# Kernel optimization log

Hardware: AMD Instinct MI355X
Metric: run time of the kernel (lower is better)

## Reference

```python
import jax, jax.numpy as jnp
import numpy as np

EPS = 1e-10
LN_EPS = 1e-5
NEG = -1e30
H = 8  # attention_head


def _layernorm(x, g, b):
    mu = jnp.mean(x, axis=-1, keepdims=True)
    var = jnp.mean(jnp.square(x - mu), axis=-1, keepdims=True)
    return (x - mu) * jax.lax.rsqrt(var + LN_EPS) * g + b


def setup_inputs() -> dict:
    key = jax.random.key(0)
    ks = jax.random.split(key, 10)
    B, T, D = 4, 1024, 1024
    inputs = jax.random.normal(ks[0], (B, T, D), dtype=jnp.float32)
    lengths = jax.random.randint(ks[1], (B,), T // 2, T + 1).astype(jnp.int32)
    lengths = lengths.at[0].set(T)  # at least one full-length sequence
    noise_u = jax.random.uniform(ks[2], (B, H, T, T), dtype=jnp.float32)
    w = lambda k: (jax.random.normal(k, (D, D), dtype=jnp.float32) * 0.02)
    return {
        'inputs': inputs, 'lengths': lengths, 'noise_u': noise_u,
        'Wq': w(ks[3]), 'Wk': w(ks[4]), 'Wv': w(ks[5]),
        'Weq': w(ks[6]), 'Wek': w(ks[7]), 'Wfc': w(ks[8]),
        'bfc': jnp.zeros((D,), jnp.float32),
        'ln1_g': jnp.ones((D,), jnp.float32), 'ln1_b': jnp.zeros((D,), jnp.float32),
        'ln2_g': jnp.ones((D,), jnp.float32), 'ln2_b': jnp.zeros((D,), jnp.float32),
    }


def reference(inputs, lengths, noise_u, Wq, Wk, Wv, Weq, Wek, Wfc, bfc,
              ln1_g, ln1_b, ln2_g, ln2_b):
    B, T, D = inputs.shape
    dh = D // H
    # length mask: True where padded
    pad = jnp.arange(T)[None, :] >= lengths[:, None]            # (B, T)
    x = jnp.where(pad[:, :, None], 0.0, inputs)                  # zero padded positions

    def heads(W):
        h = x @ W.T                                              # (B,T,D)
        return h.reshape(B, T, H, dh).transpose(0, 2, 1, 3)      # (B,H,T,dh)

    q, k, v, eq, ek = (heads(W) for W in (Wq, Wk, Wv, Weq, Wek))
    scores = jnp.einsum('bhqd,bhkd->bhqk', q, k) / jnp.sqrt(jnp.float32(D))
    edge = jnp.einsum('bhqd,bhkd->bhqk', eq, ek)                 # (B,H,T,T)

    # bernoulli prior: binary-concrete sample (hard threshold), tau=1
    edges_prob = jax.nn.sigmoid(edge)
    logistic = jnp.log(noise_u + EPS) - jnp.log(1.0 - noise_u + EPS)
    y_soft = jax.nn.sigmoid(jnp.log(edges_prob + EPS) - jnp.log(1.0 - edges_prob + EPS) + logistic)
    gate = y_soft > 0.5                                          # hard edges (condition only, as in torch .data)

    valid = gate & (~pad[:, None, None, :])                      # gate AND key-length mask
    s = jnp.where(valid, scores, NEG)
    attn = jax.nn.softmax(s, axis=-1)
    attn = jnp.where(jnp.any(valid, axis=-1, keepdims=True), attn, 0.0)  # nan->0 for fully-masked rows

    ctx = jax.nn.relu(jnp.einsum('bhqk,bhkd->bhqd', attn, v))
    ctx = ctx.transpose(0, 2, 1, 3).reshape(B, T, D)

    h1 = _layernorm(ctx + x, ln1_g, ln1_b)
    h2 = jax.nn.relu(h1 @ Wfc.T + bfc) + h1
    out = _layernorm(h2, ln2_g, ln2_b)
    out = jnp.where(pad[:, :, None], 0.0, out)
    return out, attn, edges_prob
```

## Files before the change

### kernel.cpp

```cpp
#include <hip/hip_runtime.h>
#include <math.h>

constexpr int Bn = 4, Tn = 1024, Dn = 1024, Hn = 8, DH = 128;
constexpr float EPSF = 1e-10f;
constexpr float LN_EPSF = 1e-5f;
constexpr float NEGF = -1e30f;

typedef __attribute__((ext_vector_type(8))) short bf16x8;
typedef __attribute__((ext_vector_type(4))) float f32x4;
typedef __attribute__((ext_vector_type(4))) unsigned uint4v;

#define MFMA16(a, b, c) __builtin_amdgcn_mfma_f32_16x16x32_bf16(a, b, c, 0, 0, 0)

__device__ __forceinline__ short f2bf(float f) {
    unsigned u = __builtin_bit_cast(unsigned, f);
    u += 0x7fffu + ((u >> 16) & 1u);
    return (short)(u >> 16);
}
__device__ __forceinline__ float bf2f(short h) {
    return __builtin_bit_cast(float, ((unsigned)(unsigned short)h) << 16);
}
__device__ __forceinline__ unsigned pack2(float a, float b) {
    return ((unsigned)(unsigned short)f2bf(a)) | (((unsigned)(unsigned short)f2bf(b)) << 16);
}

__device__ __forceinline__ void gload16(const void* g, void* l) {
    __builtin_amdgcn_global_load_lds((__attribute__((address_space(1))) void*)g,
                                     (__attribute__((address_space(3))) void*)l,
                                     16, 0, 0);
}

template <int NW>
__device__ __forceinline__ void stage_b(const short* g, int ld, short* lds, int lane, int wid) {
#pragma unroll
    for (int s = 0; s < 8 / NW; ++s) {
        const int ii = wid * (8 / NW) + s;
        const int c = ii * 64 + lane;
        const int kb = c >> 7, r = c & 127;
        gload16(g + (size_t)r * ld + kb * 8, lds + ii * 512);
    }
}

template <int NW>
__device__ __forceinline__ void stage_f(const float* g, int ld, float* lds, int lane, int wid) {
#pragma unroll
    for (int s = 0; s < 16 / NW; ++s) {
        const int ii = wid * (16 / NW) + s;
        const int c = ii * 64 + lane;
        const int kb = c >> 8, half = (c >> 7) & 1, r = c & 127;
        gload16(g + (size_t)r * ld + kb * 8 + half * 4, lds + ii * 256);
    }
}

__device__ __forceinline__ bf16x8 fragb(const short* lds, int kbl, int r) {
    return *reinterpret_cast<const bf16x8*>(lds + kbl * 1024 + r * 8);
}

__device__ __forceinline__ bf16x8 fragf(const float* lds, int kbl, int r) {
    const f32x4 lo = *reinterpret_cast<const f32x4*>(lds + kbl * 1024 + r * 4);
    const f32x4 hi = *reinterpret_cast<const f32x4*>(lds + kbl * 1024 + 512 + r * 4);
    uint4v p;
    p[0] = pack2(lo[0], lo[1]);
    p[1] = pack2(lo[2], lo[3]);
    p[2] = pack2(hi[0], hi[1]);
    p[3] = pack2(hi[2], hi[3]);
    return __builtin_bit_cast(bf16x8, p);
}

struct CvtP { const float* src[6]; short* hi; short* lo; };

__global__ __launch_bounds__(256) void cvt_w(CvtP p) {
    const int i = blockIdx.x * 256 + threadIdx.x;
    const int mat = i >> 17;
    const int off = (i & 131071) * 8;
    const float* s = p.src[mat] + off;
    const float4 a = *reinterpret_cast<const float4*>(s);
    const float4 b = *reinterpret_cast<const float4*>(s + 4);
    const float va[8] = {a.x, a.y, a.z, a.w, b.x, b.y, b.z, b.w};
    bf16x8 h, l;
#pragma unroll
    for (int j = 0; j < 8; ++j) {
        h[j] = f2bf(va[j]);
        l[j] = f2bf(va[j] - bf2f(h[j]));
    }
    *reinterpret_cast<bf16x8*>(p.hi + (size_t)mat * 1048576 + off) = h;
    if (mat >= 3)
        *reinterpret_cast<bf16x8*>(p.lo + (size_t)(mat - 3) * 1048576 + off) = l;
}

__global__ __launch_bounds__(256) void mask_x(const float4* __restrict__ in,
                                              const int* __restrict__ lengths,
                                              short* __restrict__ xhi,
                                              short* __restrict__ xlo) {
    const int i = blockIdx.x * 256 + threadIdx.x;
    const int row = i >> 8;
    const int t = row & 1023, b = row >> 10;
    float4 v = in[i];
    if (t >= lengths[b]) { v.x = 0.f; v.y = 0.f; v.z = 0.f; v.w = 0.f; }
    short4 h, l;
    h.x = f2bf(v.x); h.y = f2bf(v.y); h.z = f2bf(v.z); h.w = f2bf(v.w);
    l.x = f2bf(v.x - bf2f(h.x)); l.y = f2bf(v.y - bf2f(h.y));
    l.z = f2bf(v.z - bf2f(h.z)); l.w = f2bf(v.w - bf2f(h.w));
    *reinterpret_cast<short4*>(xhi + (size_t)i * 4) = h;
    *reinterpret_cast<short4*>(xlo + (size_t)i * 4) = l;
}

struct ProjP { const short* whi[5]; const short* wlo[2]; short* o[5]; short* olo[2]; };

__global__ __launch_bounds__(256) void proj_mfma(const short* __restrict__ Xh,
                                                 const short* __restrict__ Xl, ProjP p) {
    __shared__ alignas(16) short T0[4096];
    __shared__ alignas(16) short T1[4096];
    __shared__ alignas(16) short T2[4096];
    __shared__ alignas(16) short T3[4096];
    const int z = blockIdx.z;
    const short* __restrict__ Wh = p.whi[z];
    const int m0 = blockIdx.y << 7, n0 = blockIdx.x << 7;
    const int tid = threadIdx.x, lane = tid & 63, wid = tid >> 6;
    const int wm = (wid >> 1) << 6, wn = (wid & 1) << 6;
    const int kbl = lane >> 4, rl = lane & 15, rw = (lane >> 4) << 2;
    f32x4 acc[4][4] = {};
    if (z < 3) {
        for (int k0 = 0; k0 < Dn; k0 += 32) {
            stage_b<4>(Xh + (size_t)m0 * Dn + k0, Dn, T0, lane, wid);
            stage_b<4>(Wh + (size_t)n0 * Dn + k0, Dn, T1, lane, wid);
            __syncthreads();
            bf16x8 a[4], b[4];
#pragma unroll
            for (int f = 0; f < 4; ++f) {
                a[f] = fragb(T0, kbl, wm + f * 16 + rl);
                b[f] = fragb(T1, kbl, wn + f * 16 + rl);
            }
#pragma unroll
            for (int i = 0; i < 4; ++i)
#pragma unroll
                for (int j = 0; j < 4; ++j)
                    acc[i][j] = MFMA16(a[i], b[j], acc[i][j]);
            __syncthreads();
        }
    } else {
        const short* __restrict__ Wl = p.wlo[z - 3];
        for (int k0 = 0; k0 < Dn; k0 += 32) {
            stage_b<4>(Xh + (size_t)m0 * Dn + k0, Dn, T0, lane, wid);
            stage_b<4>(Xl + (size_t)m0 * Dn + k0, Dn, T1, lane, wid);
            stage_b<4>(Wh + (size_t)n0 * Dn + k0, Dn, T2, lane, wid);
            stage_b<4>(Wl + (size_t)n0 * Dn + k0, Dn, T3, lane, wid);
            __syncthreads();
            bf16x8 ah[4], al[4], bh[4], bl[4];
#pragma unroll
            for (int f = 0; f < 4; ++f) {
                ah[f] = fragb(T0, kbl, wm + f * 16 + rl);
                al[f] = fragb(T1, kbl, wm + f * 16 + rl);
                bh[f] = fragb(T2, kbl, wn + f * 16 + rl);
                bl[f] = fragb(T3, kbl, wn + f * 16 + rl);
            }
#pragma unroll
            for (int i = 0; i < 4; ++i)
#pragma unroll
                for (int j = 0; j < 4; ++j) {
                    acc[i][j] = MFMA16(al[i], bh[j], acc[i][j]);
                    acc[i][j] = MFMA16(ah[i], bl[j], acc[i][j]);
                    acc[i][j] = MFMA16(ah[i], bh[j], acc[i][j]);
                }
            __syncthreads();
        }
    }
    short* __restrict__ O = p.o[z];
    short* __restrict__ OL = (z >= 3) ? p.olo[z - 3] : nullptr;
#pragma unroll
    for (int i = 0; i < 4; ++i)
#pragma unroll
        for (int r = 0; r < 4; ++r) {
            const int m = m0 + wm + i * 16 + rw + r;
            const int b = m >> 10, t = m & 1023;
#pragma unroll
            for (int j = 0; j < 4; ++j) {
                const int n = n0 + wn + j * 16 + rl;
                const int h = n >> 7, d = n & 127;
                const float av = acc[i][j][r];
                if (z == 2) {
                    O[(((size_t)(b * Hn + h) * DH + d) << 10) + t] = f2bf(av);
                } else {
                    const size_t idx = (((size_t)(b * Hn + h)) << 10 | t) * DH + d;
                    const short hi = f2bf(av);
                    O[idx] = hi;
                    if (z >= 3) OL[idx] = f2bf(av - bf2f(hi));
                }
            }
        }
}

__global__ __launch_bounds__(256) void scores_edge(
    const short* __restrict__ Q, const short* __restrict__ Kb,
    const short* __restrict__ EQh, const short* __restrict__ EQl,
    const short* __restrict__ EKh, const short* __restrict__ EKl,
    const float* __restrict__ U, const int* __restrict__ lens,
    float* __restrict__ S, float* __restrict__ EP) {
    __shared__ alignas(16) short T0[4096];
    __shared__ alignas(16) short T1[4096];
    __shared__ alignas(16) short T2[4096];
    __shared__ alignas(16) short T3[4096];
    const int z = blockIdx.z;
    const int len = lens[z >> 3];
    const int m0 = blockIdx.y << 7, n0 = blockIdx.x << 7;
    const int tid = threadIdx.x, lane = tid & 63, wid = tid >> 6;
    const int wm = (wid >> 1) << 6, wn = (wid & 1) << 6;
    const int kbl = lane >> 4, rl = lane & 15, rw = (lane >> 4) << 2;
    const size_t zo = (size_t)z << 17;

    f32x4 acce[4][4] = {};
    for (int k0 = 0; k0 < DH; k0 += 32) {
        stage_b<4>(EQh + zo + (size_t)m0 * DH + k0, DH, T0, lane, wid);
        stage_b<4>(EQl + zo + (size_t)m0 * DH + k0, DH, T1, lane, wid);
        stage_b<4>(EKh + zo + (size_t)n0 * DH + k0, DH, T2, lane, wid);
        stage_b<4>(EKl + zo + (size_t)n0 * DH + k0, DH, T3, lane, wid);
        __syncthreads();
        bf16x8 ah[4], al[4], bh[4], bl[4];
#pragma unroll
        for (int f = 0; f < 4; ++f) {
            ah[f] = fragb(T0, kbl, wm + f * 16 + rl);
            al[f] = fragb(T1, kbl, wm + f * 16 + rl);
            bh[f] = fragb(T2, kbl, wn + f * 16 + rl);
            bl[f] = fragb(T3, kbl, wn + f * 16 + rl);
        }
#pragma unroll
        for (int i = 0; i < 4; ++i)
#pragma unroll
            for (int j = 0; j < 4; ++j) {
                acce[i][j] = MFMA16(al[i], bl[j], acce[i][j]);
                acce[i][j] = MFMA16(al[i], bh[j], acce[i][j]);
                acce[i][j] = MFMA16(ah[i], bl[j], acce[i][j]);
                acce[i][j] = MFMA16(ah[i], bh[j], acce[i][j]);
            }
        __syncthreads();
    }

    f32x4 accs[4][4] = {};
    for (int k0 = 0; k0 < DH; k0 += 32) {
        stage_b<4>(Q + zo + (size_t)m0 * DH + k0, DH, T0, lane, wid);
        stage_b<4>(Kb + zo + (size_t)n0 * DH + k0, DH, T1, lane, wid);
        __syncthreads();
        bf16x8 a[4], b[4];
#pragma unroll
        for (int f = 0; f < 4; ++f) {
            a[f] = fragb(T0, kbl, wm + f * 16 + rl);
            b[f] = fragb(T1, kbl, wn + f * 16 + rl);
        }
#pragma unroll
        for (int i = 0; i < 4; ++i)
#pragma unroll
            for (int j = 0; j < 4; ++j)
                accs[i][j] = MFMA16(a[i], b[j], accs[i][j]);
        __syncthreads();
    }

#pragma unroll
    for (int i = 0; i < 4; ++i)
#pragma unroll
        for (int r = 0; r < 4; ++r) {
            const int m = m0 + wm + i * 16 + rw + r;
#pragma unroll
            for (int j = 0; j < 4; ++j) {
                const int n = n0 + wn + j * 16 + rl;
                const size_t idx = ((size_t)z << 20) + ((size_t)m << 10) + n;
                const float e = acce[i][j][r];
                EP[idx] = 1.f / (1.f + __expf(-e));
                const float u = U[idx];
                const float zz = e + __logf(u + EPSF) - __logf(1.f - u + EPSF);
                const bool valid = (zz > 0.f) && (n < len);
                S[idx] = valid ? accs[i][j][r] * (1.f / 32.f) : NEGF;
            }
        }
}

__global__ __launch_bounds__(512) void softmax_ctx(float* __restrict__ P,
                                                   const short* __restrict__ Vt,
                                                   float* __restrict__ C) {
    __shared__ alignas(16) float Ps[4096];
    __shared__ alignas(16) short Vs[4096];
    const int z = blockIdx.y;
    const int bb = z >> 3, h = z & 7;
    const int m0 = blockIdx.x << 7;
    const int tid = threadIdx.x, lane = tid & 63, wid = tid >> 6;

    {
        const int r = tid >> 2, qd = tid & 3;
        float* rowp = P + ((size_t)z << 20) + ((size_t)(m0 + r) << 10) + qd * 8;
        float mrun = -3.0e38f, lrun = 0.f;
#pragma unroll 8
        for (int c = 0; c < 32; ++c) {
            const float4 v0 = *reinterpret_cast<const float4*>(rowp + c * 32);
            const float4 v1 = *reinterpret_cast<const float4*>(rowp + c * 32 + 4);
            const float cm = fmaxf(fmaxf(fmaxf(v0.x, v0.y), fmaxf(v0.z, v0.w)),
                                   fmaxf(fmaxf(v1.x, v1.y), fmaxf(v1.z, v1.w)));
            const float mn = fmaxf(mrun, cm);
            lrun = lrun * __expf(mrun - mn) +
                   __expf(v0.x - mn) + __expf(v0.y - mn) +
                   __expf(v0.z - mn) + __expf(v0.w - mn) +
                   __expf(v1.x - mn) + __expf(v1.y - mn) +
                   __expf(v1.z - mn) + __expf(v1.w - mn);
            mrun = mn;
        }
#pragma unroll
        for (int off = 1; off <= 2; off <<= 1) {
            const float mo = __shfl_xor(mrun, off);
            const float lo2 = __shfl_xor(lrun, off);
            const float mn = fmaxf(mrun, mo);
            lrun = lrun * __expf(mrun - mn) + lo2 * __expf(mo - mn);
            mrun = mn;
        }
        const float inv = (mrun > -5e29f) ? 1.f / lrun : 0.f;
#pragma unroll 8
        for (int c = 0; c < 32; ++c) {
            float4 v0 = *reinterpret_cast<const float4*>(rowp + c * 32);
            float4 v1 = *reinterpret_cast<const float4*>(rowp + c * 32 + 4);
            v0.x = __expf(v0.x - mrun) * inv; v0.y = __expf(v0.y - mrun) * inv;
            v0.z = __expf(v0.z - mrun) * inv; v0.w = __expf(v0.w - mrun) * inv;
            v1.x = __expf(v1.x - mrun) * inv; v1.y = __expf(v1.y - mrun) * inv;
            v1.z = __expf(v1.z - mrun) * inv; v1.w = __expf(v1.w - mrun) * inv;
            *reinterpret_cast<float4*>(rowp + c * 32) = v0;
            *reinterpret_cast<float4*>(rowp + c * 32 + 4) = v1;
        }
    }
    __syncthreads();

    const int wm = (wid >> 2) << 6, wn = (wid & 3) << 5;
    const int kbl = lane >> 4, rl = lane & 15, rw = (lane >> 4) << 2;
    f32x4 acc[4][2] = {};
    for (int k0 = 0; k0 < Tn; k0 += 32) {
        stage_f<8>(P + ((size_t)z << 20) + ((size_t)m0 << 10) + k0, Tn, Ps, lane, wid);
        stage_b<8>(Vt + ((size_t)z << 17) + k0, Tn, Vs, lane, wid);
        __syncthreads();
        bf16x8 a[4], b[2];
#pragma unroll
        for (int f = 0; f < 4; ++f) a[f] = fragf(Ps, kbl, wm + f * 16 + rl);
#pragma unroll
        for (int f = 0; f < 2; ++f) b[f] = fragb(Vs, kbl, wn + f * 16 + rl);
#pragma unroll
        for (int i = 0; i < 4; ++i)
#pragma unroll
            for (int j = 0; j < 2; ++j)
                acc[i][j] = MFMA16(a[i], b[j], acc[i][j]);
        __syncthreads();
    }
#pragma unroll
    for (int i = 0; i < 4; ++i)
#pragma unroll
        for (int r = 0; r < 4; ++r) {
            const int m = m0 + wm + i * 16 + rw + r;
#pragma unroll
            for (int j = 0; j < 2; ++j) {
                const int n = wn + j * 16 + rl;
                C[(((size_t)(bb << 10 | m)) << 10) + h * DH + n] = fmaxf(acc[i][j][r], 0.f);
            }
        }
}

__global__ __launch_bounds__(256) void ln1_kernel(const float* __restrict__ ctx,
                                                  const float* __restrict__ inputs,
                                                  const int* __restrict__ lengths,
                                                  const float* __restrict__ g,
                                                  const float* __restrict__ bb,
                                                  float* __restrict__ h1f,
                                                  short* __restrict__ h1hi,
                                                  short* __restrict__ h1lo) {
    __shared__ float red1[4];
    __shared__ float red2[4];
    const int row = blockIdx.x;
    const int t = row & 1023, b = row >> 10;
    const bool live = t < lengths[b];
    const size_t base = (size_t)row * Dn;
    const int tid = threadIdx.x;
    float4 v = reinterpret_cast<const float4*>(ctx + base)[tid];
    if (live) {
        const float4 r = reinterpret_cast<const float4*>(inputs + base)[tid];
        v.x += r.x; v.y += r.y; v.z += r.z; v.w += r.w;
    }
    float s = v.x + v.y + v.z + v.w;
#pragma unroll
    for (int off = 32; off >= 1; off >>= 1) s += __shfl_xor(s, off);
    if ((tid & 63) == 0) red1[tid >> 6] = s;
    __syncthreads();
    const float mu = (red1[0] + red1[1] + red1[2] + red1[3]) * (1.f / Dn);
    const float d0 = v.x - mu, d1 = v.y - mu, d2 = v.z - mu, d3 = v.w - mu;
    float sq = d0 * d0 + d1 * d1 + d2 * d2 + d3 * d3;
#pragma unroll
    for (int off = 32; off >= 1; off >>= 1) sq += __shfl_xor(sq, off);
    if ((tid & 63) == 0) red2[tid >> 6] = sq;
    __syncthreads();
    const float var = (red2[0] + red2[1] + red2[2] + red2[3]) * (1.f / Dn);
    const float rstd = rsqrtf(var + LN_EPSF);
    const float4 gv = reinterpret_cast<const float4*>(g)[tid];
    const float4 bv = reinterpret_cast<const float4*>(bb)[tid];
    float4 ov;
    ov.x = d0 * rstd * gv.x + bv.x;
    ov.y = d1 * rstd * gv.y + bv.y;
    ov.z = d2 * rstd * gv.z + bv.z;
    ov.w = d3 * rstd * gv.w + bv.w;
    reinterpret_cast<float4*>(h1f + base)[tid] = ov;
    short4 hs, ls;
    hs.x = f2bf(ov.x); hs.y = f2bf(ov.y); hs.z = f2bf(ov.z); hs.w = f2bf(ov.w);
    ls.x = f2bf(ov.x - bf2f(hs.x)); ls.y = f2bf(ov.y - bf2f(hs.y));
    ls.z = f2bf(ov.z - bf2f(hs.z)); ls.w = f2bf(ov.w - bf2f(hs.w));
    reinterpret_cast<short4*>(h1hi + base)[tid] = hs;
    reinterpret_cast<short4*>(h1lo + base)[tid] = ls;
}

__global__ __launch_bounds__(512) void fc_mfma(const short* __restrict__ Xh,
                                               const short* __restrict__ Xl,
                                               const short* __restrict__ Wh,
                                               const short* __restrict__ Wl,
                                               const float* __restrict__ bias,
                                               const float* __restrict__ H1f,
                                               float* __restrict__ O) {
    __shared__ alignas(16) short T0[4096];
    __shared__ alignas(16) short T1[4096];
    __shared__ alignas(16) short T2[4096];
    __shared__ alignas(16) short T3[4096];
    const int m0 = blockIdx.y << 7, n0 = blockIdx.x << 7;
    const int tid = threadIdx.x, lane = tid & 63, wid = tid >> 6;
    const int wm = (wid >> 2) << 6, wn = (wid & 3) << 5;
    const int kbl = lane >> 4, rl = lane & 15, rw = (lane >> 4) << 2;
    f32x4 acc[4][2] = {};
    for (int k0 = 0; k0 < Dn; k0 += 32) {
        stage_b<8>(Xh + (size_t)m0 * Dn + k0, Dn, T0, lane, wid);
        stage_b<8>(Xl + (size_t)m0 * Dn + k0, Dn, T1, lane, wid);
        stage_b<8>(Wh + (size_t)n0 * Dn + k0, Dn, T2, lane, wid);
        stage_b<8>(Wl + (size_t)n0 * Dn + k0, Dn, T3, lane, wid);
        __syncthreads();
        bf16x8 ah[4], al[4], bh[2], bl[2];
#pragma unroll
        for (int f = 0; f < 4; ++f) {
            ah[f] = fragb(T0, kbl, wm + f * 16 + rl);
            al[f] = fragb(T1, kbl, wm + f * 16 + rl);
        }
#pragma unroll
        for (int f = 0; f < 2; ++f) {
            bh[f] = fragb(T2, kbl, wn + f * 16 + rl);
            bl[f] = fragb(T3, kbl, wn + f * 16 + rl);
        }
#pragma unroll
        for (int i = 0; i < 4; ++i)
#pragma unroll
            for (int j = 0; j < 2; ++j) {
                acc[i][j] = MFMA16(al[i], bh[j], acc[i][j]);
                acc[i][j] = MFMA16(ah[i], bl[j], acc[i][j]);
                acc[i][j] = MFMA16(ah[i], bh[j], acc[i][j]);
            }
        __syncthreads();
    }
#pragma unroll
    for (int i = 0; i < 4; ++i)
#pragma unroll
        for (int r = 0; r < 4; ++r) {
            const int m = m0 + wm + i * 16 + rw + r;
#pragma unroll
            for (int j = 0; j < 2; ++j) {
                const int n = n0 + wn + j * 16 + rl;
                const size_t idx = ((size_t)m << 10) + n;
                O[idx] = fmaxf(acc[i][j][r] + bias[n], 0.f) + H1f[idx];
            }
        }
}

__global__ __launch_bounds__(256) void ln2_kernel(const float* __restrict__ a,
                                                  const float* __restrict__ g,
                                                  const float* __restrict__ bb,
                                                  const int* __restrict__ lengths,
                                                  float* __restrict__ o) {
    __shared__ float red1[4];
    __shared__ float red2[4];
    const int row = blockIdx.x;
    const size_t base = (size_t)row * Dn;
    const int tid = threadIdx.x;
    float4 v = reinterpret_cast<const float4*>(a + base)[tid];
    float s = v.x + v.y + v.z + v.w;
#pragma unroll
    for (int off = 32; off >= 1; off >>= 1) s += __shfl_xor(s, off);
    if ((tid & 63) == 0) red1[tid >> 6] = s;
    __syncthreads();
    const float mu = (red1[0] + red1[1] + red1[2] + red1[3]) * (1.f / Dn);
    const float d0 = v.x - mu, d1 = v.y - mu, d2 = v.z - mu, d3 = v.w - mu;
    float sq = d0 * d0 + d1 * d1 + d2 * d2 + d3 * d3;
#pragma unroll
    for (int off = 32; off >= 1; off >>= 1) sq += __shfl_xor(sq, off);
    if ((tid & 63) == 0) red2[tid >> 6] = sq;
    __syncthreads();
    const float var = (red2[0] + red2[1] + red2[2] + red2[3]) * (1.f / Dn);
    const float rstd = rsqrtf(var + LN_EPSF);
    const float4 gv = reinterpret_cast<const float4*>(g)[tid];
    const float4 bv = reinterpret_cast<const float4*>(bb)[tid];
    float4 ov;
    ov.x = d0 * rstd * gv.x + bv.x;
    ov.y = d1 * rstd * gv.y + bv.y;
    ov.z = d2 * rstd * gv.z + bv.z;
    ov.w = d3 * rstd * gv.w + bv.w;
    const int t = row & 1023, b = row >> 10;
    if (t >= lengths[b]) { ov.x = 0.f; ov.y = 0.f; ov.z = 0.f; ov.w = 0.f; }
    reinterpret_cast<float4*>(o + base)[tid] = ov;
}

extern "C" void kernel_launch(void* const* d_in, const int* in_sizes, int n_in,
                              void* d_out, int out_size, void* d_ws, size_t ws_size,
                              hipStream_t stream) {
    const float* inputs = (const float*)d_in[0];
    const int* lengths = (const int*)d_in[1];
    const float* noise = (const float*)d_in[2];
    const float* bfc = (const float*)d_in[9];
    const float* ln1_g = (const float*)d_in[10];
    const float* ln1_b = (const float*)d_in[11];
    const float* ln2_g = (const float*)d_in[12];
    const float* ln2_b = (const float*)d_in[13];

    float* out = (float*)d_out;
    float* attn = out + (size_t)Bn * Tn * Dn;
    float* ep = attn + (size_t)Bn * Hn * Tn * Tn;

    constexpr size_t MB = 1u << 20;
    char* W = (char*)d_ws;
    short* xhi = (short*)(W + 0 * MB);
    short* xlo = (short*)(W + 8 * MB);
    short* whi = (short*)(W + 16 * MB);
    short* wlo = (short*)(W + 28 * MB);
    short* qb = (short*)(W + 34 * MB);
    short* kb = (short*)(W + 42 * MB);
    short* vtb = (short*)(W + 50 * MB);
    short* eqh = (short*)(W + 58 * MB);
    short* eql = (short*)(W + 66 * MB);
    short* ekh = (short*)(W + 74 * MB);
    short* ekl = (short*)(W + 82 * MB);
    float* ctx = (float*)(W + 58 * MB);
    float* h1f = (float*)(W + 74 * MB);
    short* h1hi = (short*)(W + 34 * MB);
    short* h1lo = (short*)(W + 42 * MB);
    float* h2 = (float*)(W + 0 * MB);

    CvtP cp;
    for (int j = 0; j < 6; ++j) cp.src[j] = (const float*)d_in[3 + j];
    cp.hi = whi; cp.lo = wlo;
    cvt_w<<<dim3(3072), 256, 0, stream>>>(cp);

    mask_x<<<dim3(4096), 256, 0, stream>>>((const float4*)inputs, lengths, xhi, xlo);

    ProjP pp;
    for (int j = 0; j < 5; ++j) pp.whi[j] = whi + (size_t)j * 1048576;
    pp.wlo[0] = wlo;
    pp.wlo[1] = wlo + 1048576;
    pp.o[0] = qb; pp.o[1] = kb; pp.o[2] = vtb; pp.o[3] = eqh; pp.o[4] = ekh;
    pp.olo[0] = eql; pp.olo[1] = ekl;
    proj_mfma<<<dim3(8, 32, 5), 256, 0, stream>>>(xhi, xlo, pp);

    scores_edge<<<dim3(8, 8, 32), 256, 0, stream>>>(qb, kb, eqh, eql, ekh, ekl,
                                                    noise, lengths, attn, ep);

    softmax_ctx<<<dim3(8, 32), 512, 0, stream>>>(attn, vtb, ctx);

    ln1_kernel<<<dim3(Bn * Tn), 256, 0, stream>>>(ctx, inputs, lengths, ln1_g, ln1_b,
                                                  h1f, h1hi, h1lo);

    fc_mfma<<<dim3(8, 32), 512, 0, stream>>>(h1hi, h1lo, whi + 5 * 1048576,
                                             wlo + 2 * 1048576, bfc, h1f, h2);

    ln2_kernel<<<dim3(Bn * Tn), 256, 0, stream>>>(h2, ln2_g, ln2_b, lengths, out);
}
```

Measured before the change: 516.8 us.

## Split projection kernel, deepen K tiles to 64, and fuse score/edge GEMM loops

Splits the single projection launch into a plain bf16 kernel for Q/K/V and a 512-thread split-precision kernel for the edge projections, which removes the divergent branch and balances work per block. The projection and FC GEMMs now stage 64-wide K slices, halving barrier and loop overhead per K step at the cost of twice the LDS. The scores_edge kernel merges its edge and score K loops into one loop and drops the lo*lo MFMA term from the edge product, trading a little precision for fewer MFMAs and barriers. The larger LDS footprint may reduce occupancy.

```diff
diff --git a/kernel.cpp b/kernel.cpp
--- a/kernel.cpp
+++ b/kernel.cpp
@@ -38,6 +38,18 @@
         const int c = ii * 64 + lane;
         const int kb = c >> 7, r = c & 127;
         gload16(g + (size_t)r * ld + kb * 8, lds + ii * 512);
+    }
+}
+
+template <int NT>
+__device__ __forceinline__ void stage64(const short* g, int ld, short* lds, int lane, int wid) {
+    constexpr int IT = 1024 / NT;
+#pragma unroll
+    for (int s = 0; s < IT; ++s) {
+        const int cb = wid * IT + s;
+        const int c = cb * 64 + lane;
+        const int kb = c >> 7, r = c & 127;
+        gload16(g + (size_t)r * ld + kb * 8, lds + cb * 512);
     }
 }
 
@@ -105,68 +117,106 @@
     *reinterpret_cast<short4*>(xlo + (size_t)i * 4) = l;
 }
 
-struct ProjP { const short* whi[5]; const short* wlo[2]; short* o[5]; short* olo[2]; };
-
-__global__ __launch_bounds__(256) void proj_mfma(const short* __restrict__ Xh,
-                                                 const short* __restrict__ Xl, ProjP p) {
-    __shared__ alignas(16) short T0[4096];
-    __shared__ alignas(16) short T1[4096];
-    __shared__ alignas(16) short T2[4096];
-    __shared__ alignas(16) short T3[4096];
+struct Proj3P { const short* w[3]; short* o[3]; };
+
+__global__ __launch_bounds__(256) void proj3_mfma(const short* __restrict__ Xh, Proj3P p) {
+    __shared__ alignas(16) short T0[8192];
+    __shared__ alignas(16) short T1[8192];
     const int z = blockIdx.z;
-    const short* __restrict__ Wh = p.whi[z];
+    const short* __restrict__ Wh = p.w[z];
     const int m0 = blockIdx.y << 7, n0 = blockIdx.x << 7;
     const int tid = threadIdx.x, lane = tid & 63, wid = tid >> 6;
     const int wm = (wid >> 1) << 6, wn = (wid & 1) << 6;
     const int kbl = lane >> 4, rl = lane & 15, rw = (lane >> 4) << 2;
     f32x4 acc[4][4] = {};
-    if (z < 3) {
-        for (int k0 = 0; k0 < Dn; k0 += 32) {
-            stage_b<4>(Xh + (size_t)m0 * Dn + k0, Dn, T0, lane, wid);
-            stage_b<4>(Wh + (size_t)n0 * Dn + k0, Dn, T1, lane, wid);
-            __syncthreads();
+    for (int k0 = 0; k0 < Dn; k0 += 64) {
+        stage64<256>(Xh + (size_t)m0 * Dn + k0, Dn, T0, lane, wid);
+        stage64<256>(Wh + (size_t)n0 * Dn + k0, Dn, T1, lane, wid);
+        __syncthreads();
+#pragma unroll
+        for (int hh = 0; hh < 2; ++hh) {
             bf16x8 a[4], b[4];
 #pragma unroll
             for (int f = 0; f < 4; ++f) {
-                a[f] = fragb(T0, kbl, wm + f * 16 + rl);
-                b[f] = fragb(T1, kbl, wn + f * 16 + rl);
+                a[f] = fragb(T0, hh * 4 + kbl, wm + f * 16 + rl);
+                b[f] = fragb(T1, hh * 4 + kbl, wn + f * 16 + rl);
             }
 #pragma unroll
             for (int i = 0; i < 4; ++i)
 #pragma unroll
                 for (int j = 0; j < 4; ++j)
                     acc[i][j] = MFMA16(a[i], b[j], acc[i][j]);
-            __syncthreads();
-        }
-    } else {
-        const short* __restrict__ Wl = p.wlo[z - 3];
-        for (int k0 = 0; k0 < Dn; k0 += 32) {
-            stage_b<4>(Xh + (size_t)m0 * Dn + k0, Dn, T0, lane, wid);
-            stage_b<4>(Xl + (size_t)m0 * Dn + k0, Dn, T1, lane, wid);
-            stage_b<4>(Wh + (size_t)n0 * Dn + k0, Dn, T2, lane, wid);
-            stage_b<4>(Wl + (size_t)n0 * Dn + k0, Dn, T3, lane, wid);
-            __syncthreads();
-            bf16x8 ah[4], al[4], bh[4], bl[4];
+        }
+        __syncthreads();
+    }
+    short* __restrict__ O = p.o[z];
+#pragma unroll
+    for (int i = 0; i < 4; ++i)
+#pragma unroll
+        for (int r = 0; r < 4; ++r) {
+            const int m = m0 + wm + i * 16 + rw + r;
+            const int b = m >> 10, t = m & 1023;
+#pragma unroll
+            for (int j = 0; j < 4; ++j) {
+                const int n = n0 + wn + j * 16 + rl;
+                const int h = n >> 7, d = n & 127;
+                const short val = f2bf(acc[i][j][r]);
+                if (z == 2)
+                    O[(((size_t)(b * Hn + h) * DH + d) << 10) + t] = val;
+                else
+                    O[((((size_t)(b * Hn + h)) << 10) + t) * DH + d] = val;
+            }
+        }
+}
+
+struct Proj2P { const short* wh[2]; const short* wl[2]; short* oh[2]; short* ol[2]; };
+
+__global__ __launch_bounds__(512) void proj2_mfma(const short* __restrict__ Xh,
+                                                  const short* __restrict__ Xl, Proj2P p) {
+    __shared__ alignas(16) short T0[8192];
+    __shared__ alignas(16) short T1[8192];
+    __shared__ alignas(16) short T2[8192];
+    __shared__ alignas(16) short T3[8192];
+    const int z = blockIdx.z;
+    const short* __restrict__ Wh = p.wh[z];
+    const short* __restrict__ Wl = p.wl[z];
+    const int m0 = blockIdx.y << 7, n0 = blockIdx.x << 7;
+    const int tid = threadIdx.x, lane = tid & 63, wid = tid >> 6;
+    const int wm = (wid >> 2) << 6, wn = (wid & 3) << 5;
+    const int kbl = lane >> 4, rl = lane & 15, rw = (lane >> 4) << 2;
+    f32x4 acc[4][2] = {};
+    for (int k0 = 0; k0 < Dn; k0 += 64) {
+        stage64<512>(Xh + (size_t)m0 * Dn + k0, Dn, T0, lane, wid);
+        stage64<512>(Xl + (size_t)m0 * Dn + k0, Dn, T1, lane, wid);
+        stage64<512>(Wh + (size_t)n0 * Dn + k0, Dn, T2, lane, wid);
+        stage64<512>(Wl + (size_t)n0 * Dn + k0, Dn, T3, lane, wid);
+        __syncthreads();
+#pragma unroll
+        for (int hh = 0; hh < 2; ++hh) {
+            bf16x8 ah[4], al[4], bh[2], bl[2];
 #pragma unroll
             for (int f = 0; f < 4; ++f) {
-                ah[f] = fragb(T0, kbl, wm + f * 16 + rl);
-                al[f] = fragb(T1, kbl, wm + f * 16 + rl);
-                bh[f] = fragb(T2, kbl, wn + f * 16 + rl);
-                bl[f] = fragb(T3, kbl, wn + f * 16 + rl);
+                ah[f] = fragb(T0, hh * 4 + kbl, wm + f * 16 + rl);
+                al[f] = fragb(T1, hh * 4 + kbl, wm + f * 16 + rl);
+            }
+#pragma unroll
+            for (int f = 0; f < 2; ++f) {
+                bh[f] = fragb(T2, hh * 4 + kbl, wn + f * 16 + rl);
+                bl[f] = fragb(T3, hh * 4 + kbl, wn + f * 16 + rl);
             }
 #pragma unroll
             for (int i = 0; i < 4; ++i)
 #pragma unroll
-                for (int j = 0; j < 4; ++j) {
+                for (int j = 0; j < 2; ++j) {
                     acc[i][j] = MFMA16(al[i], bh[j], acc[i][j]);
                     acc[i][j] = MFMA16(ah[i], bl[j], acc[i][j]);
                     acc[i][j] = MFMA16(ah[i], bh[j], acc[i][j]);
                 }
-            __syncthreads();
-        }
-    }
-    short* __restrict__ O = p.o[z];
-    short* __restrict__ OL = (z >= 3) ? p.olo[z - 3] : nullptr;
+        }
+        __syncthreads();
+    }
+    short* __restrict__ OH = p.oh[z];
+    short* __restrict__ OL = p.ol[z];
 #pragma unroll
     for (int i = 0; i < 4; ++i)
 #pragma unroll
@@ -174,18 +224,14 @@
             const int m = m0 + wm + i * 16 + rw + r;
             const int b = m >> 10, t = m & 1023;
 #pragma unroll
-            for (int j = 0; j < 4; ++j) {
+            for (int j = 0; j < 2; ++j) {
                 const int n = n0 + wn + j * 16 + rl;
                 const int h = n >> 7, d = n & 127;
+                const size_t idx = (((size_t)(b * Hn + h)) << 10 | t) * DH + d;
                 const float av = acc[i][j][r];
-                if (z == 2) {
-                    O[(((size_t)(b * Hn + h) * DH + d) << 10) + t] = f2bf(av);
-                } else {
-                    const size_t idx = (((size_t)(b * Hn + h)) << 10 | t) * DH + d;
-                    const short hi = f2bf(av);
-                    O[idx] = hi;
-                    if (z >= 3) OL[idx] = f2bf(av - bf2f(hi));
-                }
+                const short hi = f2bf(av);
+                OH[idx] = hi;
+                OL[idx] = f2bf(av - bf2f(hi));
             }
         }
 }
@@ -200,6 +246,8 @@
     __shared__ alignas(16) short T1[4096];
     __shared__ alignas(16) short T2[4096];
     __shared__ alignas(16) short T3[4096];
+    __shared__ alignas(16) short T4[4096];
+    __shared__ alignas(16) short T5[4096];
     const int z = blockIdx.z;
     const int len = lens[z >> 3];
     const int m0 = blockIdx.y << 7, n0 = blockIdx.x << 7;
@@ -209,48 +257,46 @@
     const size_t zo = (size_t)z << 17;
 
     f32x4 acce[4][4] = {};
+    f32x4 accs[4][4] = {};
     for (int k0 = 0; k0 < DH; k0 += 32) {
         stage_b<4>(EQh + zo + (size_t)m0 * DH + k0, DH, T0, lane, wid);
         stage_b<4>(EQl + zo + (size_t)m0 * DH + k0, DH, T1, lane, wid);
         stage_b<4>(EKh + zo + (size_t)n0 * DH + k0, DH, T2, lane, wid);
         stage_b<4>(EKl + zo + (size_t)n0 * DH + k0, DH, T3, lane, wid);
-        __syncthreads();
-        bf16x8 ah[4], al[4], bh[4], bl[4];
-#pragma unroll
-        for (int f = 0; f < 4; ++f) {
-            ah[f] = fragb(T0, kbl, wm + f * 16 + rl);
-            al[f] = fragb(T1, kbl, wm + f * 16 + rl);
-            bh[f] = fragb(T2, kbl, wn + f * 16 + rl);
-            bl[f] = fragb(T3, kbl, wn + f * 16 + rl);
-        }
-#pragma unroll
-        for (int i = 0; i < 4; ++i)
-#pragma unroll
-            for (int j = 0; j < 4; ++j) {
-                acce[i][j] = MFMA16(al[i], bl[j], acce[i][j]);
-                acce[i][j] = MFMA16(al[i], bh[j], acce[i][j]);
-                acce[i][j] = MFMA16(ah[i], bl[j], acce[i][j]);
-                acce[i][j] = MFMA16(ah[i], bh[j], acce[i][j]);
-            }
-        __syncthreads();
-    }
-
-    f32x4 accs[4][4] = {};
-    for (int k0 = 0; k0 < DH; k0 += 32) {
-        stage_b<4>(Q + zo + (size_t)m0 * DH + k0, DH, T0, lane, wid);
-        stage_b<4>(Kb + zo + (size_t)n0 * DH + k0, DH, T1, lane, wid);
-        __syncthreads();
-        bf16x8 a[4], b[4];
-#pragma unroll
-        for (int f = 0; f < 4; ++f) {
-            a[f] = fragb(T0, kbl, wm + f * 16 + rl);
-            b[f] = fragb(T1, kbl, wn + f * 16 + rl);
-        }
-#pragma unroll
-        for (int i = 0; i < 4; ++i)
-#pragma unroll
-            for (int j = 0; j < 4; ++j)
-                accs[i][j] = MFMA16(a[i], b[j], accs[i][j]);
+        stage_b<4>(Q + zo + (size_t)m0 * DH + k0, DH, T4, lane, wid);
+        stage_b<4>(Kb + zo + (size_t)n0 * DH + k0, DH, T5, lane, wid);
+        __syncthreads();
+        {
+            bf16x8 ah[4], al[4], bh[4], bl[4];
+#pragma unroll
+            for (int f = 0; f < 4; ++f) {
+                ah[f] = fragb(T0, kbl, wm + f * 16 + rl);
+                al[f] = fragb(T1, kbl, wm + f * 16 + rl);
+                bh[f] = fragb(T2, kbl, wn + f * 16 + rl);
+                bl[f] = fragb(T3, kbl, wn + f * 16 + rl);
+            }
+#pragma unroll
+            for (int i = 0; i < 4; ++i)
+#pragma unroll
+                for (int j = 0; j < 4; ++j) {
+                    acce[i][j] = MFMA16(al[i], bh[j], acce[i][j]);
+                    acce[i][j] = MFMA16(ah[i], bl[j], acce[i][j]);
+                    acce[i][j] = MFMA16(ah[i], bh[j], acce[i][j]);
+                }
+        }
+        {
+            bf16x8 a[4], b[4];
+#pragma unroll
+            for (int f = 0; f < 4; ++f) {
+                a[f] = fragb(T4, kbl, wm + f * 16 + rl);
+                b[f] = fragb(T5, kbl, wn + f * 16 + rl);
+            }
+#pragma unroll
+            for (int i = 0; i < 4; ++i)
+#pragma unroll
+                for (int j = 0; j < 4; ++j)
+                    accs[i][j] = MFMA16(a[i], b[j], accs[i][j]);
+        }
         __syncthreads();
     }
 
@@ -413,40 +459,43 @@
                                                const float* __restrict__ bias,
                                                const float* __restrict__ H1f,
                                                float* __restrict__ O) {
-    __shared__ alignas(16) short T0[4096];
-    __shared__ alignas(16) short T1[4096];
-    __shared__ alignas(16) short T2[4096];
-    __shared__ alignas(16) short T3[4096];
+    __shared__ alignas(16) short T0[8192];
+    __shared__ alignas(16) short T1[8192];
+    __shared__ alignas(16) short T2[8192];
+    __shared__ alignas(16) short T3[8192];
     const int m0 = blockIdx.y << 7, n0 = blockIdx.x << 7;
     const int tid = threadIdx.x, lane = tid & 63, wid = tid >> 6;
     const int wm = (wid >> 2) << 6, wn = (wid & 3) << 5;
     const int kbl = lane >> 4, rl = lane & 15, rw = (lane >> 4) << 2;
     f32x4 acc[4][2] = {};
-    for (int k0 = 0; k0 < Dn; k0 += 32) {
-        stage_b<8>(Xh + (size_t)m0 * Dn + k0, Dn, T0, lane, wid);
-        stage_b<8>(Xl + (size_t)m0 * Dn + k0, Dn, T1, lane, wid);
-        stage_b<8>(Wh + (size_t)n0 * Dn + k0, Dn, T2, lane, wid);
-        stage_b<8>(Wl + (size_t)n0 * Dn + k0, Dn, T3, lane, wid);
-        __syncthreads();
-        bf16x8 ah[4], al[4], bh[2], bl[2];
-#pragma unroll
-        for (int f = 0; f < 4; ++f) {
-            ah[f] = fragb(T0, kbl, wm + f * 16 + rl);
-            al[f] = fragb(T1, kbl, wm + f * 16 + rl);
-        }
-#pragma unroll
-        for (int f = 0; f < 2; ++f) {
-            bh[f] = fragb(T2, kbl, wn + f * 16 + rl);
-            bl[f] = fragb(T3, kbl, wn + f * 16 + rl);
-        }
-#pragma unroll
-        for (int i = 0; i < 4; ++i)
-#pragma unroll
-            for (int j = 0; j < 2; ++j) {
-                acc[i][j] = MFMA16(al[i], bh[j], acc[i][j]);
-                acc[i][j] = MFMA16(ah[i], bl[j], acc[i][j]);
-                acc[i][j] = MFMA16(ah[i], bh[j], acc[i][j]);
-            }
+    for (int k0 = 0; k0 < Dn; k0 += 64) {
+        stage64<512>(Xh + (size_t)m0 * Dn + k0, Dn, T0, lane, wid);
+        stage64<512>(Xl + (size_t)m0 * Dn + k0, Dn, T1, lane, wid);
+        stage64<512>(Wh + (size_t)n0 * Dn + k0, Dn, T2, lane, wid);
+        stage64<512>(Wl + (size_t)n0 * Dn + k0, Dn, T3, lane, wid);
+        __syncthreads();
+#pragma unroll
+        for (int hh = 0; hh < 2; ++hh) {
+            bf16x8 ah[4], al[4], bh[2], bl[2];
+#pragma unroll
+            for (int f = 0; f < 4; ++f) {
+                ah[f] = fragb(T0, hh * 4 + kbl, wm + f * 16 + rl);
+                al[f] = fragb(T1, hh * 4 + kbl, wm + f * 16 + rl);
+            }
+#pragma unroll
+            for (int f = 0; f < 2; ++f) {
+                bh[f] = fragb(T2, hh * 4 + kbl, wn + f * 16 + rl);
+                bl[f] = fragb(T3, hh * 4 + kbl, wn + f * 16 + rl);
+            }
+#pragma unroll
+            for (int i = 0; i < 4; ++i)
+#pragma unroll
+                for (int j = 0; j < 2; ++j) {
+                    acc[i][j] = MFMA16(al[i], bh[j], acc[i][j]);
+                    acc[i][j] = MFMA16(ah[i], bl[j], acc[i][j]);
+                    acc[i][j] = MFMA16(ah[i], bh[j], acc[i][j]);
+                }
+        }
         __syncthreads();
     }
 #pragma unroll
@@ -542,13 +591,18 @@
 
     mask_x<<<dim3(4096), 256, 0, stream>>>((const float4*)inputs, lengths, xhi, xlo);
 
-    ProjP pp;
-    for (int j = 0; j < 5; ++j) pp.whi[j] = whi + (size_t)j * 1048576;
-    pp.wlo[0] = wlo;
-    pp.wlo[1] = wlo + 1048576;
-    pp.o[0] = qb; pp.o[1] = kb; pp.o[2] = vtb; pp.o[3] = eqh; pp.o[4] = ekh;
-    pp.olo[0] = eql; pp.olo[1] = ekl;
-    proj_mfma<<<dim3(8, 32, 5), 256, 0, stream>>>(xhi, xlo, pp);
+    Proj3P p3;
+    p3.w[0] = whi;                 p3.o[0] = qb;
+    p3.w[1] = whi + 1 * 1048576;   p3.o[1] = kb;
+    p3.w[2] = whi + 2 * 1048576;   p3.o[2] = vtb;
+    proj3_mfma<<<dim3(8, 32, 3), 256, 0, stream>>>(xhi, p3);
+
+    Proj2P p2;
+    p2.wh[0] = whi + 3 * 1048576;  p2.wl[0] = wlo;
+    p2.wh[1] = whi + 4 * 1048576;  p2.wl[1] = wlo + 1048576;
+    p2.oh[0] = eqh; p2.ol[0] = eql;
+    p2.oh[1] = ekh; p2.ol[1] = ekl;
+    proj2_mfma<<<dim3(8, 32, 2), 512, 0, stream>>>(xhi, xlo, p2);
 
     scores_edge<<<dim3(8, 8, 32), 256, 0, stream>>>(qb, kb, eqh, eql, ekh, ekl,
                                                     noise, lengths, attn, ep);
```

New measurement: 564.9 us. +9.3%, slower.
